# Kernel optimization log

Hardware: AMD Instinct MI355X
Metric: run time of the kernel (lower is better)

## Reference

```python
import jax, jax.numpy as jnp
import numpy as np

B, T, H, HS, E = 4096, 32, 16, 32, 512  # T == block_size == head_size (required by the module's concat-on-time quirk)


def setup_inputs() -> dict:
    key = jax.random.key(0)
    ks = jax.random.split(key, 6)
    s_e = 1.0 / np.sqrt(E).astype(np.float32)
    s_p = 1.0 / np.sqrt(H * HS).astype(np.float32)
    return {
        "x": jax.random.normal(ks[0], (B, T, E), jnp.float32),
        "Wq": jax.random.normal(ks[1], (H, HS, E), jnp.float32) * s_e,  # per-head Linear(E->HS, no bias)
        "Wk": jax.random.normal(ks[2], (H, HS, E), jnp.float32) * s_e,
        "Wv": jax.random.normal(ks[3], (H, HS, E), jnp.float32) * s_e,
        "Wp": jax.random.normal(ks[4], (E, H * HS), jnp.float32) * s_p,  # proj: Linear(H*HS -> E)
        "bp": jnp.zeros((E,), jnp.float32),
    }


def reference(x, Wq, Wk, Wv, Wp, bp):
    # Per-head projections, batched over heads (original loops in Python).
    q = jnp.einsum('bte,hde->bhtd', x, Wq)  # [B,H,T,HS]
    k = jnp.einsum('bte,hde->bhtd', x, Wk)
    v = jnp.einsum('bte,hde->bhtd', x, Wv)
    wei = jnp.einsum('bhtd,bhsd->bhts', q, k) * (HS ** -0.5)  # [B,H,T,T]
    mask = jnp.tril(jnp.ones((T, T), bool))  # causal (T == block_size)
    wei = jnp.where(mask, wei, -jnp.inf)
    wei = jax.nn.softmax(wei, axis=-1)
    # dropout is identity in eval mode
    out = jnp.einsum('bhts,bhsd->bhtd', wei, v)  # [B,H,T,HS]
    # torch.cat(..., dim=1): stack head outputs along the TIME axis -> [B, H*T, HS]
    out = out.reshape(B, H * T, HS)
    out = jnp.swapaxes(out, 1, 2)  # [B, HS, H*T]; valid only because T == HS -> last dim == H*HS == E
    return out @ Wp.T + bp  # [B, HS, E]
```

## Files before the change

### kernel.cpp

```cpp
#include <hip/hip_runtime.h>
#include <stdint.h>

typedef __attribute__((ext_vector_type(8))) short bf16x8;
typedef __attribute__((ext_vector_type(4))) float f32x4;

#define MFMA16(a, b, c) __builtin_amdgcn_mfma_f32_16x16x32_bf16((a), (b), (c), 0, 0, 0)

__device__ __forceinline__ unsigned short f2bf(float f) {
  unsigned int b = __float_as_uint(f);
  b += 0x7FFFu + ((b >> 16) & 1u);
  return (unsigned short)(b >> 16);
}
__device__ __forceinline__ bf16x8 cvt8(const float4 a, const float4 b) {
  bf16x8 r;
  r[0] = (short)f2bf(a.x); r[1] = (short)f2bf(a.y);
  r[2] = (short)f2bf(a.z); r[3] = (short)f2bf(a.w);
  r[4] = (short)f2bf(b.x); r[5] = (short)f2bf(b.y);
  r[6] = (short)f2bf(b.z); r[7] = (short)f2bf(b.w);
  return r;
}
template <bool BF16W>
__device__ __forceinline__ bf16x8 ldw(const void* p, size_t off) {
  if constexpr (BF16W) {
    return *(const bf16x8*)((const unsigned short*)p + off);
  } else {
    const float* f = (const float*)p + off;
    return cvt8(*(const float4*)f, *(const float4*)(f + 4));
  }
}
__device__ __forceinline__ int sw(int row, int chunk) {
  return row * 512 + ((chunk ^ (row & 7)) << 3);
}

__global__ void cvt_weights_k(const float* __restrict__ wq,
                              const float* __restrict__ wk,
                              const float* __restrict__ wv,
                              const float* __restrict__ wp,
                              unsigned short* __restrict__ dst) {
  const int seg = blockIdx.x >> 7;
  const int blk = blockIdx.x & 127;
  const float* src = (seg == 0) ? wq : (seg == 1) ? wk : (seg == 2) ? wv : wp;
  unsigned short* d = dst + (size_t)seg * 262144;
  const int i = (blk * 256 + threadIdx.x) * 8;
  float4 lo = *(const float4*)&src[i];
  float4 hi = *(const float4*)&src[i + 4];
  *(bf16x8*)&d[i] = cvt8(lo, hi);
}

template <bool BF16W>
__global__ __launch_bounds__(256, 2) void qkv_attn_k(
    const float* __restrict__ x,
    const void* __restrict__ wq,
    const void* __restrict__ wk,
    const void* __restrict__ wv,
    float* __restrict__ y) {
  __shared__ __align__(16) unsigned short Xs[32 * 512];
  __shared__ __align__(16) unsigned short Scr[4][3][32 * 40];
  const int tid  = threadIdx.x;
  const int lane = tid & 63;
  const int wave = tid >> 6;
  const int m    = lane & 15;
  const int quad = lane >> 4;
  const int b    = blockIdx.x;
  const int koff = (blockIdx.x >> 3) & 15;
  const int hgo  = (blockIdx.x >> 7) & 3;

  {
    const float* xg = x + (size_t)b * (32 * 512);
#pragma unroll
    for (int i = 0; i < 8; i++) {
      int c = tid + 256 * i;
      int row = c >> 6, ch = c & 63;
      float4 lo = *(const float4*)&xg[row * 512 + ch * 8];
      float4 hi = *(const float4*)&xg[row * 512 + ch * 8 + 4];
      *(bf16x8*)&Xs[sw(row, ch)] = cvt8(lo, hi);
    }
  }
  __syncthreads();

  unsigned short* Qs = &Scr[wave][0][0];
  unsigned short* Ks = &Scr[wave][1][0];
  unsigned short* Vt = &Scr[wave][2][0];

  for (int hg = 0; hg < 4; hg++) {
    const int h = ((hg + hgo) & 3) * 4 + wave;
    f32x4 aq[2][2] = {}; f32x4 ak[2][2] = {}; f32x4 av[2][2] = {};
    const size_t wbase = (size_t)(h * 32 + m) * 512 + quad * 8;

    bf16x8 a0A, a1A, bq0A, bq1A, bk0A, bk1A, bv0A, bv1A;
    bf16x8 a0B, a1B, bq0B, bq1B, bk0B, bk1B, bv0B, bv1B;

#define LDF(S, idx) { \
    const int kx = ((idx) + koff) & 15; \
    const int kb = kx * 32; \
    a0##S  = *(const bf16x8*)&Xs[sw(m, kx * 4 + quad)]; \
    a1##S  = *(const bf16x8*)&Xs[sw(16 + m, kx * 4 + quad)]; \
    bq0##S = ldw<BF16W>(wq, wbase + kb); \
    bq1##S = ldw<BF16W>(wq, wbase + 16 * 512 + kb); \
    bk0##S = ldw<BF16W>(wk, wbase + kb); \
    bk1##S = ldw<BF16W>(wk, wbase + 16 * 512 + kb); \
    bv0##S = ldw<BF16W>(wv, wbase + kb); \
    bv1##S = ldw<BF16W>(wv, wbase + 16 * 512 + kb); }

#define MMF(S) { \
    aq[0][0] = MFMA16(a0##S, bq0##S, aq[0][0]); \
    aq[1][0] = MFMA16(a1##S, bq0##S, aq[1][0]); \
    aq[0][1] = MFMA16(a0##S, bq1##S, aq[0][1]); \
    aq[1][1] = MFMA16(a1##S, bq1##S, aq[1][1]); \
    ak[0][0] = MFMA16(a0##S, bk0##S, ak[0][0]); \
    ak[1][0] = MFMA16(a1##S, bk0##S, ak[1][0]); \
    ak[0][1] = MFMA16(a0##S, bk1##S, ak[0][1]); \
    ak[1][1] = MFMA16(a1##S, bk1##S, ak[1][1]); \
    av[0][0] = MFMA16(a0##S, bv0##S, av[0][0]); \
    av[1][0] = MFMA16(a1##S, bv0##S, av[1][0]); \
    av[0][1] = MFMA16(a0##S, bv1##S, av[0][1]); \
    av[1][1] = MFMA16(a1##S, bv1##S, av[1][1]); }

    LDF(A, 0)
    for (int i = 0; i < 14; i += 2) {
      LDF(B, i + 1)
      MMF(A)
      LDF(A, i + 2)
      MMF(B)
    }
    LDF(B, 15)
    MMF(A)
    MMF(B)
#undef LDF
#undef MMF

#pragma unroll
    for (int mi = 0; mi < 2; mi++)
#pragma unroll
      for (int ni = 0; ni < 2; ni++)
#pragma unroll
        for (int r = 0; r < 4; r++) {
          int row = mi * 16 + quad * 4 + r;
          int col = ni * 16 + m;
          Qs[row * 40 + col] = f2bf(aq[mi][ni][r]);
          Ks[row * 40 + col] = f2bf(ak[mi][ni][r]);
          Vt[col * 40 + row] = f2bf(av[mi][ni][r]);
        }
    f32x4 sAcc[2][2];
#pragma unroll
    for (int mi = 0; mi < 2; mi++)
#pragma unroll
      for (int ni = 0; ni < 2; ni++) {
        bf16x8 qa = *(const bf16x8*)&Qs[(mi * 16 + m) * 40 + quad * 8];
        bf16x8 kb = *(const bf16x8*)&Ks[(ni * 16 + m) * 40 + quad * 8];
        f32x4 z = {};
        sAcc[mi][ni] = MFMA16(qa, kb, z);
      }
    float invs[2][4];
#pragma unroll
    for (int mi = 0; mi < 2; mi++)
#pragma unroll
      for (int r = 0; r < 4; r++) {
        int t = mi * 16 + quad * 4 + r;
        float s0 = sAcc[mi][0][r] * 0.17677669529663687f;
        float s1 = sAcc[mi][1][r] * 0.17677669529663687f;
        s0 = (m <= t) ? s0 : -1e30f;
        s1 = (16 + m <= t) ? s1 : -1e30f;
        float mx = fmaxf(s0, s1);
#pragma unroll
        for (int off = 1; off < 16; off <<= 1) mx = fmaxf(mx, __shfl_xor(mx, off));
        float e0 = __expf(s0 - mx);
        float e1 = __expf(s1 - mx);
        float sm = e0 + e1;
#pragma unroll
        for (int off = 1; off < 16; off <<= 1) sm += __shfl_xor(sm, off);
        invs[mi][r] = 1.0f / sm;
        Qs[t * 40 + m] = f2bf(e0);
        Qs[t * 40 + 16 + m] = f2bf(e1);
      }
    f32x4 oAcc[2][2];
#pragma unroll
    for (int mi = 0; mi < 2; mi++)
#pragma unroll
      for (int ni = 0; ni < 2; ni++) {
        bf16x8 pa = *(const bf16x8*)&Qs[(mi * 16 + m) * 40 + quad * 8];
        bf16x8 vb = *(const bf16x8*)&Vt[(ni * 16 + m) * 40 + quad * 8];
        f32x4 z = {};
        oAcc[mi][ni] = MFMA16(pa, vb, z);
      }
#pragma unroll
    for (int mi = 0; mi < 2; mi++)
#pragma unroll
      for (int ni = 0; ni < 2; ni++) {
        float4 o;
        o.x = oAcc[mi][ni][0] * invs[mi][0];
        o.y = oAcc[mi][ni][1] * invs[mi][1];
        o.z = oAcc[mi][ni][2] * invs[mi][2];
        o.w = oAcc[mi][ni][3] * invs[mi][3];
        int d = ni * 16 + m;
        int t0 = mi * 16 + quad * 4;
        *(float4*)&y[(size_t)b * 16384 + (size_t)d * 512 + h * 32 + t0] = o;
      }
  }
}

template <bool BF16W>
__global__ __launch_bounds__(256, 2) void proj_k(
    float* __restrict__ y,
    const void* __restrict__ wp,
    const float* __restrict__ bp) {
  __shared__ __align__(16) unsigned short Ys[64 * 512];
  const int tid  = threadIdx.x;
  const int lane = tid & 63;
  const int wave = tid >> 6;
  const int m    = lane & 15;
  const int quad = lane >> 4;
  const size_t rbase = (size_t)blockIdx.x * 64;
  const int koff = (blockIdx.x >> 3) & 15;

  {
    const float* yg = y + rbase * 512;
#pragma unroll
    for (int i = 0; i < 16; i++) {
      int c = tid + 256 * i;
      int row = c >> 6, ch = c & 63;
      float4 lo = *(const float4*)&yg[row * 512 + ch * 8];
      float4 hi = *(const float4*)&yg[row * 512 + ch * 8 + 4];
      *(bf16x8*)&Ys[sw(row, ch)] = cvt8(lo, hi);
    }
  }
  __syncthreads();

  const int nb = wave * 128;
  f32x4 acc[4][8] = {};
  bf16x8 aA[4], aB[4], wA[8], wB[8];

#define K2A(S, idx) { \
    const int kx = ((idx) + koff) & 15; \
    _Pragma("unroll") \
    for (int mi = 0; mi < 4; mi++) \
      a##S[mi] = *(const bf16x8*)&Ys[sw(mi * 16 + m, kx * 4 + quad)]; }
#define K2W(S, idx) { \
    const int kx = ((idx) + koff) & 15; \
    const int kb = kx * 32 + quad * 8; \
    _Pragma("unroll") \
    for (int ni = 0; ni < 8; ni++) \
      w##S[ni] = ldw<BF16W>(wp, (size_t)(nb + ni * 16 + m) * 512 + kb); }
#define K2MM(S) { \
    _Pragma("unroll") \
    for (int ni = 0; ni < 8; ni++) \
      _Pragma("unroll") \
      for (int mi = 0; mi < 4; mi++) \
        acc[mi][ni] = MFMA16(a##S[mi], w##S[ni], acc[mi][ni]); }

  K2A(A, 0) K2W(A, 0)
  for (int i = 0; i < 14; i += 2) {
    K2A(B, i + 1) K2W(B, i + 1)
    K2MM(A)
    K2A(A, i + 2) K2W(A, i + 2)
    K2MM(B)
  }
  K2A(B, 15) K2W(B, 15)
  K2MM(A)
  K2MM(B)
#undef K2A
#undef K2W
#undef K2MM

#pragma unroll
  for (int ni = 0; ni < 8; ni++) {
    const int col = nb + ni * 16 + m;
    const float bias = bp[col];
#pragma unroll
    for (int mi = 0; mi < 4; mi++)
#pragma unroll
      for (int r = 0; r < 4; r++) {
        size_t row = rbase + mi * 16 + quad * 4 + r;
        y[row * 512 + col] = acc[mi][ni][r] + bias;
      }
  }
}

extern "C" void kernel_launch(void* const* d_in, const int* in_sizes, int n_in,
                              void* d_out, int out_size, void* d_ws, size_t ws_size,
                              hipStream_t stream) {
  (void)in_sizes; (void)n_in; (void)out_size;
  const float* x  = (const float*)d_in[0];
  const float* wq = (const float*)d_in[1];
  const float* wk = (const float*)d_in[2];
  const float* wv = (const float*)d_in[3];
  const float* wp = (const float*)d_in[4];
  const float* bp = (const float*)d_in[5];
  float* y = (float*)d_out;

  const size_t WE = 262144;
  if (ws_size >= 4 * WE * sizeof(unsigned short)) {
    unsigned short* wb = (unsigned short*)d_ws;
    cvt_weights_k<<<512, 256, 0, stream>>>(wq, wk, wv, wp, wb);
    qkv_attn_k<true><<<4096, 256, 0, stream>>>(x, wb, wb + WE, wb + 2 * WE, y);
    proj_k<true><<<2048, 256, 0, stream>>>(y, wb + 3 * WE, bp);
  } else {
    qkv_attn_k<false><<<4096, 256, 0, stream>>>(x, wq, wk, wv, y);
    proj_k<false><<<2048, 256, 0, stream>>>(y, wp, bp);
  }
}
```

Baseline: 1.308 ms.

## Pack bf16 weights in MFMA fragment order and raise occupancy to three blocks

The weight conversion kernel now writes bf16 weights in a tiled order that matches the MFMA B-fragment layout, so each lane fetches one contiguous 16-byte chunk and a wave reads 1 KB contiguously instead of strided rows. The per-block k-offset and head-group rotation used to spread cache accesses are removed. The V scratch buffer is dropped by reusing the K buffer for transposed V after scores are computed, which cuts shared memory enough to allow launch_bounds of 3 blocks per CU. This adds register pressure risk under the tighter bound and may reintroduce cache or channel contention now that the stagger is gone.

Measured after the change: 1.430 ms. +9.3%, slower.

```diff
diff --git a/kernel.cpp b/kernel.cpp
--- a/kernel.cpp
+++ b/kernel.cpp
@@ -41,29 +41,34 @@
   const int blk = blockIdx.x & 127;
   const float* src = (seg == 0) ? wq : (seg == 1) ? wk : (seg == 2) ? wv : wp;
   unsigned short* d = dst + (size_t)seg * 262144;
-  const int i = (blk * 256 + threadIdx.x) * 8;
-  float4 lo = *(const float4*)&src[i];
-  float4 hi = *(const float4*)&src[i + 4];
-  *(bf16x8*)&d[i] = cvt8(lo, hi);
+  const int c = blk * 256 + threadIdx.x;
+  const int row = ((c >> 10) << 4) + (c & 15);
+  const int col = ((c >> 6) & 15) * 32 + ((c >> 4) & 3) * 8;
+  const float* s = src + row * 512 + col;
+  *(bf16x8*)&d[(size_t)c * 8] = cvt8(*(const float4*)s, *(const float4*)(s + 4));
+}
+
+template <bool PACKED>
+__device__ __forceinline__ size_t wbase0(int g32, int lane, int m, int quad) {
+  if constexpr (PACKED) return (size_t)g32 * 512 + (size_t)lane * 8;
+  else                  return (size_t)(g32 + m) * 512 + quad * 8;
 }
 
 template <bool BF16W>
-__global__ __launch_bounds__(256, 2) void qkv_attn_k(
+__global__ __launch_bounds__(256, 3) void qkv_attn_k(
     const float* __restrict__ x,
     const void* __restrict__ wq,
     const void* __restrict__ wk,
     const void* __restrict__ wv,
     float* __restrict__ y) {
   __shared__ __align__(16) unsigned short Xs[32 * 512];
-  __shared__ __align__(16) unsigned short Scr[4][3][32 * 40];
+  __shared__ __align__(16) unsigned short Scr[4][2][32 * 40];
   const int tid  = threadIdx.x;
   const int lane = tid & 63;
   const int wave = tid >> 6;
   const int m    = lane & 15;
   const int quad = lane >> 4;
   const int b    = blockIdx.x;
-  const int koff = (blockIdx.x >> 3) & 15;
-  const int hgo  = (blockIdx.x >> 7) & 3;
 
   {
     const float* xg = x + (size_t)b * (32 * 512);
@@ -80,27 +85,27 @@
 
   unsigned short* Qs = &Scr[wave][0][0];
   unsigned short* Ks = &Scr[wave][1][0];
-  unsigned short* Vt = &Scr[wave][2][0];
 
   for (int hg = 0; hg < 4; hg++) {
-    const int h = ((hg + hgo) & 3) * 4 + wave;
+    const int h = hg * 4 + wave;
     f32x4 aq[2][2] = {}; f32x4 ak[2][2] = {}; f32x4 av[2][2] = {};
-    const size_t wbase = (size_t)(h * 32 + m) * 512 + quad * 8;
+    const size_t wb = wbase0<BF16W>(h * 32, lane, m, quad);
+    const int kmul = BF16W ? 512 : 32;
 
     bf16x8 a0A, a1A, bq0A, bq1A, bk0A, bk1A, bv0A, bv1A;
     bf16x8 a0B, a1B, bq0B, bq1B, bk0B, bk1B, bv0B, bv1B;
 
 #define LDF(S, idx) { \
-    const int kx = ((idx) + koff) & 15; \
-    const int kb = kx * 32; \
+    const int kx = (idx); \
+    const size_t kb = (size_t)kx * kmul; \
     a0##S  = *(const bf16x8*)&Xs[sw(m, kx * 4 + quad)]; \
     a1##S  = *(const bf16x8*)&Xs[sw(16 + m, kx * 4 + quad)]; \
-    bq0##S = ldw<BF16W>(wq, wbase + kb); \
-    bq1##S = ldw<BF16W>(wq, wbase + 16 * 512 + kb); \
-    bk0##S = ldw<BF16W>(wk, wbase + kb); \
-    bk1##S = ldw<BF16W>(wk, wbase + 16 * 512 + kb); \
-    bv0##S = ldw<BF16W>(wv, wbase + kb); \
-    bv1##S = ldw<BF16W>(wv, wbase + 16 * 512 + kb); }
+    bq0##S = ldw<BF16W>(wq, wb + kb); \
+    bq1##S = ldw<BF16W>(wq, wb + 8192 + kb); \
+    bk0##S = ldw<BF16W>(wk, wb + kb); \
+    bk1##S = ldw<BF16W>(wk, wb + 8192 + kb); \
+    bv0##S = ldw<BF16W>(wv, wb + kb); \
+    bv1##S = ldw<BF16W>(wv, wb + 8192 + kb); }
 
 #define MMF(S) { \
     aq[0][0] = MFMA16(a0##S, bq0##S, aq[0][0]); \
@@ -139,7 +144,6 @@
           int col = ni * 16 + m;
           Qs[row * 40 + col] = f2bf(aq[mi][ni][r]);
           Ks[row * 40 + col] = f2bf(ak[mi][ni][r]);
-          Vt[col * 40 + row] = f2bf(av[mi][ni][r]);
         }
     f32x4 sAcc[2][2];
 #pragma unroll
@@ -173,13 +177,23 @@
         Qs[t * 40 + m] = f2bf(e0);
         Qs[t * 40 + 16 + m] = f2bf(e1);
       }
+#pragma unroll
+    for (int mi = 0; mi < 2; mi++)
+#pragma unroll
+      for (int ni = 0; ni < 2; ni++)
+#pragma unroll
+        for (int r = 0; r < 4; r++) {
+          int row = mi * 16 + quad * 4 + r;
+          int col = ni * 16 + m;
+          Ks[col * 40 + row] = f2bf(av[mi][ni][r]);
+        }
     f32x4 oAcc[2][2];
 #pragma unroll
     for (int mi = 0; mi < 2; mi++)
 #pragma unroll
       for (int ni = 0; ni < 2; ni++) {
         bf16x8 pa = *(const bf16x8*)&Qs[(mi * 16 + m) * 40 + quad * 8];
-        bf16x8 vb = *(const bf16x8*)&Vt[(ni * 16 + m) * 40 + quad * 8];
+        bf16x8 vb = *(const bf16x8*)&Ks[(ni * 16 + m) * 40 + quad * 8];
         f32x4 z = {};
         oAcc[mi][ni] = MFMA16(pa, vb, z);
       }
@@ -211,7 +225,6 @@
   const int m    = lane & 15;
   const int quad = lane >> 4;
   const size_t rbase = (size_t)blockIdx.x * 64;
-  const int koff = (blockIdx.x >> 3) & 15;
 
   {
     const float* yg = y + rbase * 512;
@@ -227,20 +240,21 @@
   __syncthreads();
 
   const int nb = wave * 128;
+  const size_t wbp = wbase0<BF16W>(nb, lane, m, quad);
+  const int kmul = BF16W ? 512 : 32;
   f32x4 acc[4][8] = {};
   bf16x8 aA[4], aB[4], wA[8], wB[8];
 
 #define K2A(S, idx) { \
-    const int kx = ((idx) + koff) & 15; \
+    const int kx = (idx); \
     _Pragma("unroll") \
     for (int mi = 0; mi < 4; mi++) \
       a##S[mi] = *(const bf16x8*)&Ys[sw(mi * 16 + m, kx * 4 + quad)]; }
 #define K2W(S, idx) { \
-    const int kx = ((idx) + koff) & 15; \
-    const int kb = kx * 32 + quad * 8; \
+    const size_t kb = (size_t)(idx) * kmul; \
     _Pragma("unroll") \
     for (int ni = 0; ni < 8; ni++) \
-      w##S[ni] = ldw<BF16W>(wp, (size_t)(nb + ni * 16 + m) * 512 + kb); }
+      w##S[ni] = ldw<BF16W>(wp, wbp + (size_t)ni * 8192 + kb); }
 #define K2MM(S) { \
     _Pragma("unroll") \
     for (int ni = 0; ni < 8; ni++) \
```
